# Optimization experiments

Hardware: AMD Instinct MI355X
Metric: run time of the kernel (lower is better)

The kernel has to match this reference:

```python
import jax, jax.numpy as jnp
import numpy as np

N, E, G = 50000, 800000, 16
IN, HID = 256, 64
NEG = 0.2  # leaky_relu negative slope used by PyG GATConv

PNAMES = ["sage_wl", "sage_bl", "sage_wr", "mlp_w1", "mlp_b1", "mlp_w2", "mlp_b2",
          "g1_w", "g1_as", "g1_ad", "g1_we", "g1_ae", "g1_b",
          "g2_w", "g2_as", "g2_ad", "g2_we", "g2_ae", "g2_b",
          "go_w", "go_as", "go_ad", "go_we", "go_ae", "go_b"]


def setup_inputs() -> dict:
    ks = iter(jax.random.split(jax.random.key(0), 40))
    def nrm(shape, s=0.05):
        return jax.random.normal(next(ks), shape, jnp.float32) * s
    inp = {
        "x": nrm((N, IN), 1.0),
        "edge_index": jax.random.randint(next(ks), (2, E), 0, N),
        "node_types": jax.random.randint(next(ks), (N,), 0, 3),
        "edge_attr": jax.random.uniform(next(ks), (E, 1), jnp.float32),
        "batch": jnp.sort(jax.random.randint(next(ks), (N,), 0, G)),
        "sage_wl": nrm((HID, IN)),
        "sage_bl": jnp.zeros((HID,), jnp.float32),
        "sage_wr": nrm((HID, IN)),
        "mlp_w1": nrm((64, 2 * HID)),
        "mlp_b1": jnp.zeros((64,), jnp.float32),
        "mlp_w2": nrm((1, 64)),
        "mlp_b2": jnp.zeros((1,), jnp.float32),
    }
    for name, h in (("g1", 2), ("g2", 2), ("go", 1)):
        inp[name + "_w"] = nrm((h * HID, HID))
        inp[name + "_as"] = nrm((h, HID))
        inp[name + "_ad"] = nrm((h, HID))
        inp[name + "_we"] = nrm((h * HID, 1))
        inp[name + "_ae"] = nrm((h, HID))
        inp[name + "_b"] = jnp.zeros((HID,), jnp.float32)
    return inp


def _gat(x, src, dst, e, W, a_s, a_d, We, a_e, b):
    # PyG GATConv (concat=False, edge_dim=1), eval mode (dropout off)
    H, C = a_s.shape
    h = (x @ W.T).reshape(N, H, C)                      # [N,H,C]
    a_edge = ((e @ We.T).reshape(-1, H, C) * a_e).sum(-1)   # [Esl,H]
    alpha = (h * a_s).sum(-1)[src] + (h * a_d).sum(-1)[dst] + a_edge
    alpha = jnp.where(alpha > 0, alpha, NEG * alpha)    # leaky_relu(0.2)
    m = jax.ops.segment_max(alpha, dst, num_segments=N)  # every node has a self-loop -> finite
    num = jnp.exp(alpha - m[dst])
    den = jax.ops.segment_sum(num, dst, num_segments=N)
    coef = num / den[dst]                               # segment softmax over incoming edges
    out = jax.ops.segment_sum(h[src] * coef[..., None], dst, num_segments=N)
    return out.mean(axis=1) + b                         # concat=False -> mean over heads


def _forward(x, edge_index, node_types, edge_attr, batch, p):
    src, dst = edge_index[0], edge_index[1]
    # SAGEConv: mean aggregation of neighbors + root transform
    deg = jax.ops.segment_sum(jnp.ones((E,), x.dtype), dst, num_segments=N)
    agg = jax.ops.segment_sum(x[src], dst, num_segments=N) / jnp.maximum(deg, 1.0)[:, None]
    h = jax.nn.relu(agg @ p["sage_wl"].T + p["sage_bl"] + x @ p["sage_wr"].T)
    # add self-loops; edge_attr for loops = per-node mean of incoming attrs (fill_value='mean')
    loop = jnp.arange(N)
    src_sl = jnp.concatenate([src, loop])
    dst_sl = jnp.concatenate([dst, loop])
    mean_e = jax.ops.segment_sum(edge_attr, dst, num_segments=N) / jnp.maximum(deg, 1.0)[:, None]
    e_sl = jnp.concatenate([edge_attr, mean_e], axis=0)
    for name in ("g1", "g2", "go"):
        h = jax.nn.relu(_gat(h, src_sl, dst_sl, e_sl,
                             p[name + "_w"], p[name + "_as"], p[name + "_ad"],
                             p[name + "_we"], p[name + "_ae"], p[name + "_b"]))
    def pool(mask):  # masked mean pool per graph
        w = mask.astype(h.dtype)
        s = jax.ops.segment_sum(h * w[:, None], batch, num_segments=G)
        c = jnp.maximum(jax.ops.segment_sum(w, batch, num_segments=G), 1.0)
        return s / c[:, None]
    readout = jnp.concatenate([pool(node_types == 1), pool(node_types == 2)], axis=1)
    hid = jax.nn.relu(readout @ p["mlp_w1"].T + p["mlp_b1"])
    return (hid @ p["mlp_w2"].T + p["mlp_b2"]).squeeze(-1)


def reference(x, edge_index, node_types, edge_attr, batch,
              sage_wl, sage_bl, sage_wr, mlp_w1, mlp_b1, mlp_w2, mlp_b2,
              g1_w, g1_as, g1_ad, g1_we, g1_ae, g1_b,
              g2_w, g2_as, g2_ad, g2_we, g2_ae, g2_b,
              go_w, go_as, go_ad, go_we, go_ae, go_b):
    vals = [sage_wl, sage_bl, sage_wr, mlp_w1, mlp_b1, mlp_w2, mlp_b2,
            g1_w, g1_as, g1_ad, g1_we, g1_ae, g1_b,
            g2_w, g2_as, g2_ad, g2_we, g2_ae, g2_b,
            go_w, go_as, go_ad, go_we, go_ae, go_b]
    return _forward(x, edge_index, node_types, edge_attr, batch, dict(zip(PNAMES, vals)))
```

## Files before the change

### kernel.cpp

```cpp
#include <hip/hip_runtime.h>
#include <hip/hip_bf16.h>

#define NN 50000
#define EE 800000
#define GG 16
#define IN_DIM 256
#define HID 64
#define NEG 0.2f
#define SCAN_NB 49
#define SMT 40

__device__ inline float wred_sum(float v) {
    for (int o = 32; o > 0; o >>= 1) v += __shfl_xor(v, o, 64);
    return v;
}
__device__ inline float wred_max(float v) {
    for (int o = 32; o > 0; o >>= 1) v = fmaxf(v, __shfl_xor(v, o, 64));
    return v;
}
__device__ inline void slot_reduce4(float4& a) {
    a.x += __shfl_xor(a.x, 16, 64); a.y += __shfl_xor(a.y, 16, 64);
    a.z += __shfl_xor(a.z, 16, 64); a.w += __shfl_xor(a.w, 16, 64);
    a.x += __shfl_xor(a.x, 32, 64); a.y += __shfl_xor(a.y, 32, 64);
    a.z += __shfl_xor(a.z, 32, 64); a.w += __shfl_xor(a.w, 32, 64);
}

__device__ inline float lrelu(float a) { return a > 0.f ? a : NEG * a; }

__global__ __launch_bounds__(256) void deg_kernel(const int* __restrict__ ei,
                                                  const float* __restrict__ eattr,
                                                  int* __restrict__ deg,
                                                  float* __restrict__ esum) {
    int e = blockIdx.x * 256 + threadIdx.x;
    if (e >= EE) return;
    int d = ei[EE + e];
    atomicAdd(&deg[d], 1);
    atomicAdd(&esum[d], eattr[e]);
}

__global__ __launch_bounds__(1024) void scan1_kernel(const int* __restrict__ deg,
                                                     int* __restrict__ row_off,
                                                     int* __restrict__ bsum) {
    __shared__ int buf[1024];
    int b = blockIdx.x;
    int i = b * 1024 + threadIdx.x;
    int v = (i < NN) ? deg[i] : 0;
    buf[threadIdx.x] = v;
    __syncthreads();
    for (int ofs = 1; ofs < 1024; ofs <<= 1) {
        int t = (threadIdx.x >= ofs) ? buf[threadIdx.x - ofs] : 0;
        __syncthreads();
        buf[threadIdx.x] += t;
        __syncthreads();
    }
    if (i < NN) row_off[i] = buf[threadIdx.x] - v;
    if (threadIdx.x == 1023) bsum[b] = buf[1023];
}

__global__ __launch_bounds__(64) void scan2_kernel(const int* __restrict__ bsum,
                                                   int* __restrict__ boff,
                                                   int* __restrict__ row_off) {
    int l = threadIdx.x;
    int v = (l < SCAN_NB) ? bsum[l] : 0;
    int incl = v;
    for (int ofs = 1; ofs < 64; ofs <<= 1) {
        int t = __shfl_up(incl, ofs, 64);
        if (l >= ofs) incl += t;
    }
    if (l < SCAN_NB) boff[l] = incl - v;
    if (l == 63) row_off[NN] = incl;
}

__global__ __launch_bounds__(1024) void scan3_kernel(const int* __restrict__ deg,
                                                     const float* __restrict__ esum,
                                                     const int* __restrict__ boff,
                                                     int* __restrict__ row_off,
                                                     int* __restrict__ pos,
                                                     float* __restrict__ mean_e,
                                                     float* __restrict__ inv_deg) {
    int b = blockIdx.x;
    int i = b * 1024 + threadIdx.x;
    if (i >= NN) return;
    int ro = row_off[i] + boff[b];
    row_off[i] = ro;
    pos[i] = ro;
    float idg = 1.0f / fmaxf((float)deg[i], 1.0f);
    inv_deg[i] = idg;
    mean_e[i] = esum[i] * idg;
}

__global__ __launch_bounds__(256) void fill_kernel(const int* __restrict__ ei,
                                                   const float* __restrict__ eattr,
                                                   int* __restrict__ pos,
                                                   int* __restrict__ csr_src,
                                                   float* __restrict__ csr_e) {
    int e = blockIdx.x * 256 + threadIdx.x;
    if (e >= EE) return;
    int d = ei[EE + e];
    int p = atomicAdd(&pos[d], 1);
    csr_src[p] = ei[e];
    csr_e[p] = eattr[e];
}

__global__ void transpose2_kernel(const float* __restrict__ wl,
                                  const float* __restrict__ wr,
                                  float* __restrict__ wtp) {
    int k = blockIdx.x;
    int j = threadIdx.x;
    float v = (j < 64) ? wl[j * 256 + k] : wr[(j - 64) * 256 + k];
    wtp[(k >> 2) * 512 + j * 4 + (k & 3)] = v;
}

__global__ void transpose_gat_kernel(const float* __restrict__ w,
                                     const float* __restrict__ a_s,
                                     const float* __restrict__ a_d,
                                     const float* __restrict__ we,
                                     const float* __restrict__ ae,
                                     float* __restrict__ wtgp,
                                     float* __restrict__ asw,
                                     float* __restrict__ adw,
                                     float* __restrict__ wedot, int H64) {
    int k = blockIdx.x;
    int j = threadIdx.x;
    if (j >= H64) return;
    int h = j >> 6;
    int c = j & 63;
    float wv = w[j * 64 + k];
    wtgp[(k >> 2) * (H64 * 4) + j * 4 + (k & 3)] = wv;
    float sv = wred_sum(wv * a_s[j]);
    float dv = wred_sum(wv * a_d[j]);
    if (c == 0) {
        asw[h * 64 + k] = sv;
        adw[h * 64 + k] = dv;
    }
    if (k == 0) {
        float wd = wred_sum(we[j] * ae[j]);
        if (c == 0) wedot[h] = wd;
    }
}

__global__ __launch_bounds__(256) void sage_mm_kernel(const float* __restrict__ x,
                                                      const float* __restrict__ wtp,
                                                      float* __restrict__ xl,
                                                      float* __restrict__ xr) {
    __shared__ float xs[SMT * 256];
    int node0 = blockIdx.x * SMT;
    const float4* x4 = (const float4*)(x + (size_t)node0 * 256);
    float4* xs4 = (float4*)xs;
    for (int t = threadIdx.x; t < SMT * 64; t += 256) xs4[t] = x4[t];
    __syncthreads();
    int jj = threadIdx.x & 63;
    int g = threadIdx.x >> 6;
    float accL[10], accR[10];
#pragma unroll
    for (int n = 0; n < 10; n++) { accL[n] = 0.f; accR[n] = 0.f; }
    for (int k4 = 0; k4 < 64; k4++) {
        const float4 wL = *(const float4*)&wtp[k4 * 512 + jj * 4];
        const float4 wR = *(const float4*)&wtp[k4 * 512 + (jj + 64) * 4];
#pragma unroll
        for (int n = 0; n < 10; n++) {
            const float4 xv = xs4[(g * 10 + n) * 64 + k4];
            accL[n] = fmaf(xv.x, wL.x, accL[n]);
            accL[n] = fmaf(xv.y, wL.y, accL[n]);
            accL[n] = fmaf(xv.z, wL.z, accL[n]);
            accL[n] = fmaf(xv.w, wL.w, accL[n]);
            accR[n] = fmaf(xv.x, wR.x, accR[n]);
            accR[n] = fmaf(xv.y, wR.y, accR[n]);
            accR[n] = fmaf(xv.z, wR.z, accR[n]);
            accR[n] = fmaf(xv.w, wR.w, accR[n]);
        }
    }
#pragma unroll
    for (int n = 0; n < 10; n++) {
        int node = node0 + g * 10 + n;
        xl[(size_t)node * 64 + jj] = accL[n];
        xr[(size_t)node * 64 + jj] = accR[n];
    }
}

template <int H>
__global__ __launch_bounds__(256) void proj_mm_kernel(const float* __restrict__ hin,
                                                      const float* __restrict__ wtgp,
                                                      float* __restrict__ hproj) {
    __shared__ float xs[SMT * 64];
    int node0 = blockIdx.x * SMT;
    const float4* h4 = (const float4*)(hin + (size_t)node0 * 64);
    float4* xs4 = (float4*)xs;
    for (int t = threadIdx.x; t < SMT * 16; t += 256) xs4[t] = h4[t];
    __syncthreads();
    int jj = threadIdx.x & 63;
    int g = threadIdx.x >> 6;
    float acc[H][10];
#pragma unroll
    for (int h = 0; h < H; h++)
#pragma unroll
        for (int n = 0; n < 10; n++) acc[h][n] = 0.f;
#pragma unroll 4
    for (int k4 = 0; k4 < 16; k4++) {
        float4 wv[H];
#pragma unroll
        for (int h = 0; h < H; h++)
            wv[h] = *(const float4*)&wtgp[k4 * (H * 256) + (h * 64 + jj) * 4];
#pragma unroll
        for (int n = 0; n < 10; n++) {
            const float4 xv = xs4[(g * 10 + n) * 16 + k4];
#pragma unroll
            for (int h = 0; h < H; h++) {
                acc[h][n] = fmaf(xv.x, wv[h].x, acc[h][n]);
                acc[h][n] = fmaf(xv.y, wv[h].y, acc[h][n]);
                acc[h][n] = fmaf(xv.z, wv[h].z, acc[h][n]);
                acc[h][n] = fmaf(xv.w, wv[h].w, acc[h][n]);
            }
        }
    }
#pragma unroll
    for (int h = 0; h < H; h++)
#pragma unroll
        for (int n = 0; n < 10; n++)
            hproj[(size_t)(node0 + g * 10 + n) * (H * 64) + h * 64 + jj] = acc[h][n];
}

__global__ __launch_bounds__(256) void attval_kernel(const float* __restrict__ hin,
                                                     const float* __restrict__ asw,
                                                     const float* __restrict__ adw,
                                                     float* __restrict__ sval,
                                                     float* __restrict__ dval, int H) {
    int wid = (blockIdx.x * 256 + threadIdx.x) >> 6;
    int lane = threadIdx.x & 63;
    if (wid >= NN) return;
    float hv = hin[(size_t)wid * 64 + lane];
    for (int h = 0; h < H; ++h) {
        float sv = wred_sum(hv * asw[h * 64 + lane]);
        float dv = wred_sum(hv * adw[h * 64 + lane]);
        if (lane == 0) {
            sval[wid * H + h] = sv;
            dval[wid * H + h] = dv;
        }
    }
}

__global__ __launch_bounds__(256) void sage_agg_kernel(const float* __restrict__ xl,
                                                       const float* __restrict__ xr,
                                                       const float* __restrict__ bl,
                                                       const float* __restrict__ inv_deg,
                                                       const int* __restrict__ row_off,
                                                       const int* __restrict__ csr_src,
                                                       float* __restrict__ hout) {
    int wid = blockIdx.x * 4 + (threadIdx.x >> 6);
    int lane = threadIdx.x & 63;
    if (wid >= NN) return;
    int slot = lane >> 4;
    int c4 = lane & 15;
    int r0 = row_off[wid], r1 = row_off[wid + 1];
    float4 acc = make_float4(0.f, 0.f, 0.f, 0.f);
#pragma unroll 4
    for (int idx = r0 + slot; idx < r1; idx += 4) {
        int s = csr_src[idx];
        const float4 hp = *(const float4*)&xl[(size_t)s * 64 + c4 * 4];
        acc.x += hp.x; acc.y += hp.y; acc.z += hp.z; acc.w += hp.w;
    }
    slot_reduce4(acc);
    if (slot == 0) {
        float idg = inv_deg[wid];
        const float4 b4 = *(const float4*)&bl[c4 * 4];
        const float4 xr4 = *(const float4*)&xr[(size_t)wid * 64 + c4 * 4];
        float4 v;
        v.x = fmaxf(acc.x * idg + b4.x + xr4.x, 0.f);
        v.y = fmaxf(acc.y * idg + b4.y + xr4.y, 0.f);
        v.z = fmaxf(acc.z * idg + b4.z + xr4.z, 0.f);
        v.w = fmaxf(acc.w * idg + b4.w + xr4.w, 0.f);
        *(float4*)&hout[(size_t)wid * 64 + c4 * 4] = v;
    }
}

__global__ __launch_bounds__(256) void gat_kernel(const float* __restrict__ hproj,
                                                  const float* __restrict__ sval,
                                                  const float* __restrict__ dval,
                                                  const float* __restrict__ wedot_buf,
                                                  const float* __restrict__ bias,
                                                  const float* __restrict__ mean_e,
                                                  const int* __restrict__ row_off,
                                                  const int* __restrict__ csr_src,
                                                  const float* __restrict__ csr_e,
                                                  float* __restrict__ hout, int H) {
    int wid = blockIdx.x * 4 + (threadIdx.x >> 6);
    int lane = threadIdx.x & 63;
    if (wid >= NN) return;
    int slot = lane >> 4;
    int c4 = lane & 15;
    int H64 = H * 64;
    int r0 = row_off[wid], r1 = row_off[wid + 1];
    float me = mean_e[wid];
    float4 acc = make_float4(0.f, 0.f, 0.f, 0.f);
    for (int h = 0; h < H; ++h) {
        float wedot = wedot_buf[h];
        float dv = dval[wid * H + h];
        float a_self = lrelu(sval[wid * H + h] + dv + me * wedot);
        float m_l = -INFINITY, den_l = 0.f;
        for (int idx = r0 + lane; idx < r1; idx += 64) {
            int s = csr_src[idx];
            float a = lrelu(sval[s * H + h] + dv + csr_e[idx] * wedot);
            float mn = fmaxf(m_l, a);
            den_l = den_l * __expf(m_l - mn) + __expf(a - mn);
            m_l = mn;
        }
        float m = fmaxf(wred_max(m_l), a_self);
        float den = wred_sum(den_l * __expf(m_l - m)) + __expf(a_self - m);
        float inv_den = 1.0f / den;
#pragma unroll 4
        for (int idx = r0 + slot; idx < r1; idx += 4) {
            int s = csr_src[idx];
            float a = lrelu(sval[s * H + h] + dv + csr_e[idx] * wedot);
            float c = __expf(a - m) * inv_den;
            const float4 hp = *(const float4*)&hproj[(size_t)s * H64 + h * 64 + c4 * 4];
            acc.x = fmaf(c, hp.x, acc.x);
            acc.y = fmaf(c, hp.y, acc.y);
            acc.z = fmaf(c, hp.z, acc.z);
            acc.w = fmaf(c, hp.w, acc.w);
        }
        if (slot == 0) {
            float c = __expf(a_self - m) * inv_den;
            const float4 hp = *(const float4*)&hproj[(size_t)wid * H64 + h * 64 + c4 * 4];
            acc.x = fmaf(c, hp.x, acc.x);
            acc.y = fmaf(c, hp.y, acc.y);
            acc.z = fmaf(c, hp.z, acc.z);
            acc.w = fmaf(c, hp.w, acc.w);
        }
    }
    slot_reduce4(acc);
    if (slot == 0) {
        float invH = 1.0f / (float)H;
        const float4 b4 = *(const float4*)&bias[c4 * 4];
        float4 v;
        v.x = fmaxf(acc.x * invH + b4.x, 0.f);
        v.y = fmaxf(acc.y * invH + b4.y, 0.f);
        v.z = fmaxf(acc.z * invH + b4.z, 0.f);
        v.w = fmaxf(acc.w * invH + b4.w, 0.f);
        *(float4*)&hout[(size_t)wid * 64 + c4 * 4] = v;
    }
}

__global__ __launch_bounds__(256) void pool_kernel(const float* __restrict__ h,
                                                   const int* __restrict__ ntype,
                                                   const int* __restrict__ batch,
                                                   float* __restrict__ pool,
                                                   float* __restrict__ cnt) {
    int nwaves = gridDim.x * 4;
    int wid = blockIdx.x * 4 + (threadIdx.x >> 6);
    int lane = threadIdx.x & 63;
    int chunk = (NN + nwaves - 1) / nwaves;
    int n0 = wid * chunk;
    int n1 = min(n0 + chunk, NN);
    if (n0 >= NN) return;
    float acc1 = 0.f, acc2 = 0.f;
    int c1 = 0, c2 = 0;
    int cur_g = batch[n0];
    for (int n = n0; n < n1; ++n) {
        int g = batch[n];
        if (g != cur_g) {
            if (c1) {
                atomicAdd(&pool[(0 * GG + cur_g) * 64 + lane], acc1);
                if (lane == 0) atomicAdd(&cnt[0 * GG + cur_g], (float)c1);
            }
            if (c2) {
                atomicAdd(&pool[(1 * GG + cur_g) * 64 + lane], acc2);
                if (lane == 0) atomicAdd(&cnt[1 * GG + cur_g], (float)c2);
            }
            acc1 = acc2 = 0.f;
            c1 = c2 = 0;
            cur_g = g;
        }
        int t = ntype[n];
        if (t == 1) { acc1 += h[n * 64 + lane]; c1++; }
        else if (t == 2) { acc2 += h[n * 64 + lane]; c2++; }
    }
    if (c1) {
        atomicAdd(&pool[(0 * GG + cur_g) * 64 + lane], acc1);
        if (lane == 0) atomicAdd(&cnt[0 * GG + cur_g], (float)c1);
    }
    if (c2) {
        atomicAdd(&pool[(1 * GG + cur_g) * 64 + lane], acc2);
        if (lane == 0) atomicAdd(&cnt[1 * GG + cur_g], (float)c2);
    }
}

__global__ __launch_bounds__(256) void mlp_kernel(const float* __restrict__ pool,
                                                  const float* __restrict__ cnt,
                                                  const float* __restrict__ w1,
                                                  const float* __restrict__ b1,
                                                  const float* __restrict__ w2,
                                                  const float* __restrict__ b2,
                                                  float* __restrict__ out) {
    __shared__ float ro[GG * 128];
    __shared__ float hid[GG * 64];
    int tid = threadIdx.x;
    for (int t = tid; t < GG * 128; t += 256) {
        int g = t >> 7;
        int j = t & 127;
        int part = j >> 6;
        float c = fmaxf(cnt[part * GG + g], 1.0f);
        ro[t] = pool[(part * GG + g) * 64 + (j & 63)] / c;
    }
    __syncthreads();
    for (int t = tid; t < GG * 64; t += 256) {
        int g = t >> 6;
        int i = t & 63;
        float s = b1[i];
        for (int j = 0; j < 128; j++) s = fmaf(ro[g * 128 + j], w1[i * 128 + j], s);
        hid[t] = fmaxf(s, 0.f);
    }
    __syncthreads();
    if (tid < GG) {
        float s = b2[0];
        for (int i = 0; i < 64; i++) s = fmaf(hid[tid * 64 + i], w2[i], s);
        out[tid] = s;
    }
}

extern "C" void kernel_launch(void* const* d_in, const int* in_sizes, int n_in,
                              void* d_out, int out_size, void* d_ws, size_t ws_size,
                              hipStream_t stream) {
    const float* x       = (const float*)d_in[0];
    const int*   ei      = (const int*)d_in[1];
    const int*   ntype   = (const int*)d_in[2];
    const float* eattr   = (const float*)d_in[3];
    const int*   batch   = (const int*)d_in[4];
    const float* sage_wl = (const float*)d_in[5];
    const float* sage_bl = (const float*)d_in[6];
    const float* sage_wr = (const float*)d_in[7];
    const float* mlp_w1  = (const float*)d_in[8];
    const float* mlp_b1  = (const float*)d_in[9];
    const float* mlp_w2  = (const float*)d_in[10];
    const float* mlp_b2  = (const float*)d_in[11];
    const float* gw[3]  = {(const float*)d_in[12], (const float*)d_in[18], (const float*)d_in[24]};
    const float* gas[3] = {(const float*)d_in[13], (const float*)d_in[19], (const float*)d_in[25]};
    const float* gad[3] = {(const float*)d_in[14], (const float*)d_in[20], (const float*)d_in[26]};
    const float* gwe[3] = {(const float*)d_in[15], (const float*)d_in[21], (const float*)d_in[27]};
    const float* gae[3] = {(const float*)d_in[16], (const float*)d_in[22], (const float*)d_in[28]};
    const float* gb[3]  = {(const float*)d_in[17], (const float*)d_in[23], (const float*)d_in[29]};

    char* base = (char*)d_ws;
    size_t o = 0;
    auto alloc = [&](size_t bytes) -> char* {
        char* p = base + o;
        o = (o + bytes + 255) & ~(size_t)255;
        return p;
    };
    int*   deg     = (int*)  alloc(NN * 4);
    float* esum    = (float*)alloc(NN * 4);
    float* mean_e  = (float*)alloc(NN * 4);
    float* inv_deg = (float*)alloc(NN * 4);
    int*   row_off = (int*)  alloc((NN + 1) * 4);
    int*   pos     = (int*)  alloc(NN * 4);
    int*   bsum    = (int*)  alloc(64 * 4);
    int*   boff    = (int*)  alloc(64 * 4);
    int*   csr_src = (int*)  alloc((size_t)EE * 4);
    float* csr_e   = (float*)alloc((size_t)EE * 4);
    float* xl      = (float*)alloc((size_t)NN * 64 * 4);
    float* xr      = (float*)alloc((size_t)NN * 64 * 4);
    float* hA      = (float*)alloc((size_t)NN * 64 * 4);
    float* hB      = (float*)alloc((size_t)NN * 64 * 4);
    float* hproj   = (float*)alloc((size_t)NN * 128 * 4);
    float* sval    = (float*)alloc((size_t)NN * 2 * 4);
    float* dval    = (float*)alloc((size_t)NN * 2 * 4);
    float* wt      = (float*)alloc(256 * 128 * 4);
    float* wtg     = (float*)alloc(64 * 128 * 4);
    float* asw     = (float*)alloc(128 * 4);
    float* adw     = (float*)alloc(128 * 4);
    float* wedot   = (float*)alloc(2 * 4);
    float* pools   = (float*)alloc(2 * GG * 64 * 4);
    float* cnt     = (float*)alloc(2 * GG * 4);

    hipMemsetAsync(deg, 0, NN * 4, stream);
    hipMemsetAsync(esum, 0, NN * 4, stream);
    hipMemsetAsync(pools, 0, 2 * GG * 64 * 4, stream);
    hipMemsetAsync(cnt, 0, 2 * GG * 4, stream);

    deg_kernel<<<EE / 256, 256, 0, stream>>>(ei, eattr, deg, esum);
    scan1_kernel<<<SCAN_NB, 1024, 0, stream>>>(deg, row_off, bsum);
    scan2_kernel<<<1, 64, 0, stream>>>(bsum, boff, row_off);
    scan3_kernel<<<SCAN_NB, 1024, 0, stream>>>(deg, esum, boff, row_off, pos, mean_e, inv_deg);
    fill_kernel<<<EE / 256, 256, 0, stream>>>(ei, eattr, pos, csr_src, csr_e);

    transpose2_kernel<<<256, 128, 0, stream>>>(sage_wl, sage_wr, wt);
    sage_mm_kernel<<<NN / SMT, 256, 0, stream>>>(x, wt, xl, xr);
    sage_agg_kernel<<<NN / 4, 256, 0, stream>>>(xl, xr, sage_bl, inv_deg, row_off, csr_src, hA);

    float* hin = hA;
    float* hout = hB;
    for (int L = 0; L < 3; ++L) {
        int H = (L == 2) ? 1 : 2;
        int H64 = H * 64;
        transpose_gat_kernel<<<64, 128, 0, stream>>>(gw[L], gas[L], gad[L], gwe[L], gae[L],
                                                     wtg, asw, adw, wedot, H64);
        if (H == 2)
            proj_mm_kernel<2><<<NN / SMT, 256, 0, stream>>>(hin, wtg, hproj);
        else
            proj_mm_kernel<1><<<NN / SMT, 256, 0, stream>>>(hin, wtg, hproj);
        attval_kernel<<<NN / 4, 256, 0, stream>>>(hin, asw, adw, sval, dval, H);
        gat_kernel<<<NN / 4, 256, 0, stream>>>(hproj, sval, dval, wedot, gb[L],
                                               mean_e, row_off, csr_src, csr_e, hout, H);
        float* tmp = hin; hin = hout; hout = tmp;
    }
    pool_kernel<<<512, 256, 0, stream>>>(hin, ntype, batch, pools, cnt);
    mlp_kernel<<<1, 256, 0, stream>>>(pools, cnt, mlp_w1, mlp_b1, mlp_w2, mlp_b2, (float*)d_out);
}
```

Before: 615.0 us.

## Skip final GAT layer for unpooled node types and merge weight prep kernels

Builds a compacted list of nodes whose type is 1 or 2, and has the last GAT layer compute outputs only for those nodes, since only they feed the masked pooling. All weight transposes and attention-vector folds for SAGE and the three GAT layers now happen in one kernel launch. The memsets are merged into two, and an unroll pragma is dropped from the GAT aggregation loop. The atomic-based selection list is built in nondeterministic order, and unpooled rows of the final output are left stale, which is safe only because pooling masks them out.

```diff
diff --git a/kernel.cpp b/kernel.cpp
--- a/kernel.cpp
+++ b/kernel.cpp
@@ -36,6 +36,18 @@
     int d = ei[EE + e];
     atomicAdd(&deg[d], 1);
     atomicAdd(&esum[d], eattr[e]);
+}
+
+__global__ __launch_bounds__(256) void build_sel_kernel(const int* __restrict__ ntype,
+                                                        int* __restrict__ nodesel,
+                                                        int* __restrict__ nsel) {
+    int n = blockIdx.x * 256 + threadIdx.x;
+    if (n >= NN) return;
+    int t = ntype[n];
+    if (t == 1 || t == 2) {
+        int p = atomicAdd(nsel, 1);
+        nodesel[p] = n;
+    }
 }
 
 __global__ __launch_bounds__(1024) void scan1_kernel(const int* __restrict__ deg,
@@ -102,40 +114,58 @@
     csr_e[p] = eattr[e];
 }
 
-__global__ void transpose2_kernel(const float* __restrict__ wl,
-                                  const float* __restrict__ wr,
-                                  float* __restrict__ wtp) {
-    int k = blockIdx.x;
+__global__ __launch_bounds__(128) void weights_kernel(const float* __restrict__ wl,
+                                                      const float* __restrict__ wr,
+                                                      float* __restrict__ wtp,
+                                                      const float* __restrict__ w0,
+                                                      const float* __restrict__ as0,
+                                                      const float* __restrict__ ad0,
+                                                      const float* __restrict__ we0,
+                                                      const float* __restrict__ ae0,
+                                                      const float* __restrict__ w1,
+                                                      const float* __restrict__ as1,
+                                                      const float* __restrict__ ad1,
+                                                      const float* __restrict__ we1,
+                                                      const float* __restrict__ ae1,
+                                                      const float* __restrict__ w2,
+                                                      const float* __restrict__ as2,
+                                                      const float* __restrict__ ad2,
+                                                      const float* __restrict__ we2,
+                                                      const float* __restrict__ ae2,
+                                                      float* __restrict__ wtg3,
+                                                      float* __restrict__ asw3,
+                                                      float* __restrict__ adw3,
+                                                      float* __restrict__ wedot3) {
+    int b = blockIdx.x;
     int j = threadIdx.x;
-    float v = (j < 64) ? wl[j * 256 + k] : wr[(j - 64) * 256 + k];
-    wtp[(k >> 2) * 512 + j * 4 + (k & 3)] = v;
-}
-
-__global__ void transpose_gat_kernel(const float* __restrict__ w,
-                                     const float* __restrict__ a_s,
-                                     const float* __restrict__ a_d,
-                                     const float* __restrict__ we,
-                                     const float* __restrict__ ae,
-                                     float* __restrict__ wtgp,
-                                     float* __restrict__ asw,
-                                     float* __restrict__ adw,
-                                     float* __restrict__ wedot, int H64) {
-    int k = blockIdx.x;
-    int j = threadIdx.x;
+    if (b < 256) {
+        int k = b;
+        float v = (j < 64) ? wl[j * 256 + k] : wr[(j - 64) * 256 + k];
+        wtp[(k >> 2) * 512 + j * 4 + (k & 3)] = v;
+        return;
+    }
+    int L = (b - 256) >> 6;
+    int k = (b - 256) & 63;
+    const float* w  = (L == 0) ? w0  : (L == 1) ? w1  : w2;
+    const float* as = (L == 0) ? as0 : (L == 1) ? as1 : as2;
+    const float* ad = (L == 0) ? ad0 : (L == 1) ? ad1 : ad2;
+    const float* we = (L == 0) ? we0 : (L == 1) ? we1 : we2;
+    const float* ae = (L == 0) ? ae0 : (L == 1) ? ae1 : ae2;
+    int H64 = (L == 2) ? 64 : 128;
     if (j >= H64) return;
     int h = j >> 6;
     int c = j & 63;
     float wv = w[j * 64 + k];
-    wtgp[(k >> 2) * (H64 * 4) + j * 4 + (k & 3)] = wv;
-    float sv = wred_sum(wv * a_s[j]);
-    float dv = wred_sum(wv * a_d[j]);
+    wtg3[L * 8192 + (k >> 2) * (H64 * 4) + j * 4 + (k & 3)] = wv;
+    float sv = wred_sum(wv * as[j]);
+    float dv = wred_sum(wv * ad[j]);
     if (c == 0) {
-        asw[h * 64 + k] = sv;
-        adw[h * 64 + k] = dv;
+        asw3[L * 128 + h * 64 + k] = sv;
+        adw3[L * 128 + h * 64 + k] = dv;
     }
     if (k == 0) {
         float wd = wred_sum(we[j] * ae[j]);
-        if (c == 0) wedot[h] = wd;
+        if (c == 0) wedot3[L * 2 + h] = wd;
     }
 }
 
@@ -282,9 +312,15 @@
                                                   const int* __restrict__ row_off,
                                                   const int* __restrict__ csr_src,
                                                   const float* __restrict__ csr_e,
-                                                  float* __restrict__ hout, int H) {
+                                                  float* __restrict__ hout, int H,
+                                                  const int* __restrict__ nodesel,
+                                                  const int* __restrict__ nsel) {
     int wid = blockIdx.x * 4 + (threadIdx.x >> 6);
     int lane = threadIdx.x & 63;
+    if (nodesel) {
+        if (wid >= *nsel) return;
+        wid = nodesel[wid];
+    }
     if (wid >= NN) return;
     int slot = lane >> 4;
     int c4 = lane & 15;
@@ -307,7 +343,6 @@
         float m = fmaxf(wred_max(m_l), a_self);
         float den = wred_sum(den_l * __expf(m_l - m)) + __expf(a_self - m);
         float inv_den = 1.0f / den;
-#pragma unroll 4
         for (int idx = r0 + slot; idx < r1; idx += 4) {
             int s = csr_src[idx];
             float a = lrelu(sval[s * H + h] + dv + csr_e[idx] * wedot);
@@ -446,14 +481,17 @@
         o = (o + bytes + 255) & ~(size_t)255;
         return p;
     };
-    int*   deg     = (int*)  alloc(NN * 4);
-    float* esum    = (float*)alloc(NN * 4);
+    char*  zblock1 = alloc((2 * (size_t)NN + 1) * 4);
+    int*   deg     = (int*)zblock1;
+    float* esum    = (float*)(zblock1 + (size_t)NN * 4);
+    int*   nsel    = (int*)(zblock1 + 2 * (size_t)NN * 4);
     float* mean_e  = (float*)alloc(NN * 4);
     float* inv_deg = (float*)alloc(NN * 4);
     int*   row_off = (int*)  alloc((NN + 1) * 4);
     int*   pos     = (int*)  alloc(NN * 4);
     int*   bsum    = (int*)  alloc(64 * 4);
     int*   boff    = (int*)  alloc(64 * 4);
+    int*   nodesel = (int*)  alloc(NN * 4);
     int*   csr_src = (int*)  alloc((size_t)EE * 4);
     float* csr_e   = (float*)alloc((size_t)EE * 4);
     float* xl      = (float*)alloc((size_t)NN * 64 * 4);
@@ -464,25 +502,29 @@
     float* sval    = (float*)alloc((size_t)NN * 2 * 4);
     float* dval    = (float*)alloc((size_t)NN * 2 * 4);
     float* wt      = (float*)alloc(256 * 128 * 4);
-    float* wtg     = (float*)alloc(64 * 128 * 4);
-    float* asw     = (float*)alloc(128 * 4);
-    float* adw     = (float*)alloc(128 * 4);
-    float* wedot   = (float*)alloc(2 * 4);
-    float* pools   = (float*)alloc(2 * GG * 64 * 4);
-    float* cnt     = (float*)alloc(2 * GG * 4);
-
-    hipMemsetAsync(deg, 0, NN * 4, stream);
-    hipMemsetAsync(esum, 0, NN * 4, stream);
-    hipMemsetAsync(pools, 0, 2 * GG * 64 * 4, stream);
-    hipMemsetAsync(cnt, 0, 2 * GG * 4, stream);
-
+    float* wtg3    = (float*)alloc(3 * 8192 * 4);
+    float* asw3    = (float*)alloc(3 * 128 * 4);
+    float* adw3    = (float*)alloc(3 * 128 * 4);
+    float* wedot3  = (float*)alloc(3 * 2 * 4);
+    char*  zblock2 = alloc((2 * GG * 64 + 2 * GG) * 4);
+    float* pools   = (float*)zblock2;
+    float* cnt     = (float*)(zblock2 + 2 * GG * 64 * 4);
+
+    hipMemsetAsync(zblock1, 0, (2 * (size_t)NN + 1) * 4, stream);
+    hipMemsetAsync(zblock2, 0, (2 * GG * 64 + 2 * GG) * 4, stream);
+
+    weights_kernel<<<448, 128, 0, stream>>>(sage_wl, sage_wr, wt,
+                                            gw[0], gas[0], gad[0], gwe[0], gae[0],
+                                            gw[1], gas[1], gad[1], gwe[1], gae[1],
+                                            gw[2], gas[2], gad[2], gwe[2], gae[2],
+                                            wtg3, asw3, adw3, wedot3);
     deg_kernel<<<EE / 256, 256, 0, stream>>>(ei, eattr, deg, esum);
+    build_sel_kernel<<<(NN + 255) / 256, 256, 0, stream>>>(ntype, nodesel, nsel);
     scan1_kernel<<<SCAN_NB, 1024, 0, stream>>>(deg, row_off, bsum);
     scan2_kernel<<<1, 64, 0, stream>>>(bsum, boff, row_off);
     scan3_kernel<<<SCAN_NB, 1024, 0, stream>>>(deg, esum, boff, row_off, pos, mean_e, inv_deg);
     fill_kernel<<<EE / 256, 256, 0, stream>>>(ei, eattr, pos, csr_src, csr_e);
 
-    transpose2_kernel<<<256, 128, 0, stream>>>(sage_wl, sage_wr, wt);
     sage_mm_kernel<<<NN / SMT, 256, 0, stream>>>(x, wt, xl, xr);
     sage_agg_kernel<<<NN / 4, 256, 0, stream>>>(xl, xr, sage_bl, inv_deg, row_off, csr_src, hA);
 
@@ -490,16 +532,19 @@
     float* hout = hB;
     for (int L = 0; L < 3; ++L) {
         int H = (L == 2) ? 1 : 2;
-        int H64 = H * 64;
-        transpose_gat_kernel<<<64, 128, 0, stream>>>(gw[L], gas[L], gad[L], gwe[L], gae[L],
-                                                     wtg, asw, adw, wedot, H64);
+        const float* wtgL = wtg3 + (size_t)L * 8192;
+        const float* aswL = asw3 + L * 128;
+        const float* adwL = adw3 + L * 128;
+        const float* wedL = wedot3 + L * 2;
         if (H == 2)
-            proj_mm_kernel<2><<<NN / SMT, 256, 0, stream>>>(hin, wtg, hproj);
+            proj_mm_kernel<2><<<NN / SMT, 256, 0, stream>>>(hin, wtgL, hproj);
         else
-            proj_mm_kernel<1><<<NN / SMT, 256, 0, stream>>>(hin, wtg, hproj);
-        attval_kernel<<<NN / 4, 256, 0, stream>>>(hin, asw, adw, sval, dval, H);
-        gat_kernel<<<NN / 4, 256, 0, stream>>>(hproj, sval, dval, wedot, gb[L],
-                                               mean_e, row_off, csr_src, csr_e, hout, H);
+            proj_mm_kernel<1><<<NN / SMT, 256, 0, stream>>>(hin, wtgL, hproj);
+        attval_kernel<<<NN / 4, 256, 0, stream>>>(hin, aswL, adwL, sval, dval, H);
+        gat_kernel<<<NN / 4, 256, 0, stream>>>(hproj, sval, dval, wedL, gb[L],
+                                               mean_e, row_off, csr_src, csr_e, hout, H,
+                                               (L == 2) ? nodesel : nullptr,
+                                               (L == 2) ? nsel : nullptr);
         float* tmp = hin; hin = hout; hout = tmp;
     }
     pool_kernel<<<512, 256, 0, stream>>>(hin, ntype, batch, pools, cnt);
```

New measurement: 607.0 us. No clear change (-1.3%).
